# Kernel tuning notes

Hardware: AMD Instinct MI355X
Metric: run time of the kernel (lower is better)

Reference implementation:

```python
import jax, jax.numpy as jnp
import numpy as np

NUM_USERS = 500000
NUM_ITEMS = 500000
EMB_DIM = 64
BATCH = 16384
BN_EPS = 1e-5


def setup_inputs() -> dict:
    key = jax.random.key(0)
    ks = jax.random.split(key, 16)
    d = {}
    d["user_ids"] = jax.random.randint(ks[0], (BATCH,), 0, NUM_USERS)
    d["item_ids"] = jax.random.randint(ks[1], (BATCH,), 0, NUM_ITEMS)
    # wide layer: Linear(num_users+num_items, 1) -> weight stored as a flat vector + scalar bias
    d["wide_w"] = jax.random.normal(ks[2], (NUM_USERS + NUM_ITEMS,), jnp.float32) * 0.002
    d["wide_b"] = jnp.zeros((), jnp.float32)
    # embedding tables (init normal std=0.1 as in _init_weights)
    d["user_table"] = jax.random.normal(ks[3], (NUM_USERS, EMB_DIM), jnp.float32) * 0.1
    d["item_table"] = jax.random.normal(ks[4], (NUM_ITEMS, EMB_DIM), jnp.float32) * 0.1
    # deep MLP: 128 -> 256 -> 128 -> 64 -> 1, xavier-ish init, zero bias
    dims = [2 * EMB_DIM, 256, 128, 64]
    for i, (din, dout) in enumerate(zip(dims[:-1], dims[1:]), start=1):
        scale = float(np.sqrt(6.0 / (din + dout)))
        d[f"w{i}"] = jax.random.uniform(ks[4 + i], (din, dout), jnp.float32, -scale, scale)
        d[f"b{i}"] = jnp.zeros((dout,), jnp.float32)
        d[f"g{i}"] = jnp.ones((dout,), jnp.float32)   # BN gamma
        d[f"be{i}"] = jnp.zeros((dout,), jnp.float32)  # BN beta
    scale = float(np.sqrt(6.0 / (64 + 1)))
    d["w4"] = jax.random.uniform(ks[9], (64, 1), jnp.float32, -scale, scale)
    d["b4"] = jnp.zeros((1,), jnp.float32)
    return d


def _bn_eval(h, g, be):
    # eval-mode BatchNorm1d with running_mean=0, running_var=1
    return g * (h * (1.0 / jnp.sqrt(1.0 + BN_EPS))) + be


def reference(user_ids, item_ids, wide_w, wide_b, user_table, item_table,
              w1, b1, g1, be1, w2, b2, g2, be2, w3, b3, g3, be3, w4, b4):
    # Wide path: one_hot(user) @ W.T + one_hot(item) @ W.T + b  ==  gather + sum + bias
    wide = wide_w[user_ids] + wide_w[NUM_USERS + item_ids] + wide_b  # [B]
    # Deep path
    x = jnp.concatenate([user_table[user_ids], item_table[item_ids]], axis=1)  # [B, 128]
    for w, b, g, be in ((w1, b1, g1, be1), (w2, b2, g2, be2), (w3, b3, g3, be3)):
        x = _bn_eval(jax.nn.relu(x @ w + b), g, be)  # Linear -> ReLU -> BN (Dropout=id in eval)
    deep = (x @ w4 + b4)[:, 0]  # [B]
    return wide + deep
```

## Files before the change

### kernel.cpp

```cpp
#include <hip/hip_runtime.h>


#define NT 512
#define TS 32

constexpr int NUM_USERS = 500000;
constexpr float BN_INV = 0.9999950000374997f;

struct __align__(16) Smem {
    float xs[TS * 132];
    float h1[TS * 260];
};

#define FMA4(xk, wv, a)                      \
    do {                                     \
        (a).x = fmaf((xk), (wv).x, (a).x);   \
        (a).y = fmaf((xk), (wv).y, (a).y);   \
        (a).z = fmaf((xk), (wv).z, (a).z);   \
        (a).w = fmaf((xk), (wv).w, (a).w);   \
    } while (0)

template <int K, int KS, int N, int NS, int FS>
__device__ __forceinline__ void mlp_layer(
    const float* __restrict__ w, const float* __restrict__ bias,
    const float* __restrict__ gamma, const float* __restrict__ beta,
    const float* in_lds, float* out_lds, int t)
{
    constexpr int JG     = FS / 4;
    constexpr int SG     = 64 / JG;
    constexpr int NSLICE = N / FS;
    constexpr int SM     = TS * NSLICE / 8;
    constexpr int SPL    = SM / SG;
    constexpr int NW4    = N / 4;
    static_assert(SPL * SG == SM, "layout");

    const int wave = t >> 6, lane = t & 63;
    const int wslice = wave % NSLICE, wsamp = wave / NSLICE;
    const int jg = lane % JG, sg = lane / JG;
    const int j0 = wslice * FS + jg * 4;
    const int s0 = wsamp * SM + sg * SPL;

    float4 acc[SPL];
#pragma unroll
    for (int s = 0; s < SPL; ++s) acc[s] = make_float4(0.f, 0.f, 0.f, 0.f);

    const float4* wp = (const float4*)w + (j0 >> 2);

#pragma unroll 4
    for (int k4 = 0; k4 < K; k4 += 4) {
        float4 wv0 = wp[(k4 + 0) * NW4];
        float4 wv1 = wp[(k4 + 1) * NW4];
        float4 wv2 = wp[(k4 + 2) * NW4];
        float4 wv3 = wp[(k4 + 3) * NW4];
        float4 xv[SPL];
#pragma unroll
        for (int s = 0; s < SPL; ++s)
            xv[s] = *(const float4*)&in_lds[(s0 + s) * KS + k4];
#pragma unroll
        for (int s = 0; s < SPL; ++s) {
            FMA4(xv[s].x, wv0, acc[s]);
            FMA4(xv[s].y, wv1, acc[s]);
            FMA4(xv[s].z, wv2, acc[s]);
            FMA4(xv[s].w, wv3, acc[s]);
        }
    }

    const float4 bv = *(const float4*)&bias[j0];
    const float4 gv = *(const float4*)&gamma[j0];
    const float4 ev = *(const float4*)&beta[j0];
#pragma unroll
    for (int s = 0; s < SPL; ++s) {
        float4 o;
        o.x = fmaxf(acc[s].x + bv.x, 0.f) * (gv.x * BN_INV) + ev.x;
        o.y = fmaxf(acc[s].y + bv.y, 0.f) * (gv.y * BN_INV) + ev.y;
        o.z = fmaxf(acc[s].z + bv.z, 0.f) * (gv.z * BN_INV) + ev.z;
        o.w = fmaxf(acc[s].w + bv.w, 0.f) * (gv.w * BN_INV) + ev.w;
        *(float4*)&out_lds[(s0 + s) * NS + j0] = o;
    }
}

__global__ __launch_bounds__(NT, 4) void wd_kernel(
    const int* __restrict__ user_ids, const int* __restrict__ item_ids,
    const float* __restrict__ wide_w, const float* __restrict__ wide_b,
    const float* __restrict__ user_table, const float* __restrict__ item_table,
    const float* __restrict__ w1, const float* __restrict__ b1,
    const float* __restrict__ g1, const float* __restrict__ be1,
    const float* __restrict__ w2, const float* __restrict__ b2,
    const float* __restrict__ g2, const float* __restrict__ be2,
    const float* __restrict__ w3, const float* __restrict__ b3,
    const float* __restrict__ g3, const float* __restrict__ be3,
    const float* __restrict__ w4, const float* __restrict__ b4,
    float* __restrict__ out)
{
    __shared__ Smem sm;
    const int t = threadIdx.x;
    const int sbase = blockIdx.x * TS;

    {
        const int s = t >> 4;
        const int p = t & 15;
        const int uid = user_ids[sbase + s];
        const int iid = item_ids[sbase + s];
        float4* row = (float4*)&sm.xs[s * 132];
        row[p]      = ((const float4*)(user_table + (long)uid * 64))[p];
        row[16 + p] = ((const float4*)(item_table + (long)iid * 64))[p];
    }

    float widev = 0.0f;
    if (t < TS * 8 && (t & 7) == 0) {
        const int s = t >> 3;
        const int uid = user_ids[sbase + s];
        const int iid = item_ids[sbase + s];
        widev = wide_w[uid] + wide_w[NUM_USERS + iid] + wide_b[0];
    }
    __syncthreads();

    mlp_layer<128, 132, 256, 260, 64>(w1, b1, g1, be1, sm.xs, sm.h1, t);
    __syncthreads();
    mlp_layer<256, 260, 128, 132, 32>(w2, b2, g2, be2, sm.h1, sm.xs, t);
    __syncthreads();
    mlp_layer<128, 132,  64,  68, 32>(w3, b3, g3, be3, sm.xs, sm.h1, t);
    __syncthreads();

    if (t < TS * 8) {
        const int s = t >> 3;
        const int g = t & 7;
        const float* h = &sm.h1[s * 68 + g * 8];
        const float4 ha = *(const float4*)(h);
        const float4 hb = *(const float4*)(h + 4);
        const float4 wa = *(const float4*)(w4 + g * 8);
        const float4 wb = *(const float4*)(w4 + g * 8 + 4);
        float p = ha.x * wa.x + ha.y * wa.y + ha.z * wa.z + ha.w * wa.w
                + hb.x * wb.x + hb.y * wb.y + hb.z * wb.z + hb.w * wb.w;
        p += __shfl_down(p, 4);
        p += __shfl_down(p, 2);
        p += __shfl_down(p, 1);
        if (g == 0) out[sbase + s] = widev + p + b4[0];
    }
}

extern "C" void kernel_launch(void* const* d_in, const int* in_sizes, int n_in,
                              void* d_out, int out_size, void* d_ws, size_t ws_size,
                              hipStream_t stream) {
    (void)in_sizes; (void)n_in; (void)d_ws; (void)ws_size;
    const int*   user_ids   = (const int*)d_in[0];
    const int*   item_ids   = (const int*)d_in[1];
    const float* wide_w     = (const float*)d_in[2];
    const float* wide_b     = (const float*)d_in[3];
    const float* user_table = (const float*)d_in[4];
    const float* item_table = (const float*)d_in[5];
    const float* w1 = (const float*)d_in[6];
    const float* b1 = (const float*)d_in[7];
    const float* g1 = (const float*)d_in[8];
    const float* be1 = (const float*)d_in[9];
    const float* w2 = (const float*)d_in[10];
    const float* b2 = (const float*)d_in[11];
    const float* g2 = (const float*)d_in[12];
    const float* be2 = (const float*)d_in[13];
    const float* w3 = (const float*)d_in[14];
    const float* b3 = (const float*)d_in[15];
    const float* g3 = (const float*)d_in[16];
    const float* be3 = (const float*)d_in[17];
    const float* w4 = (const float*)d_in[18];
    const float* b4 = (const float*)d_in[19];
    float* out = (float*)d_out;

    const int grid = 16384 / TS;
    wd_kernel<<<grid, NT, 0, stream>>>(
        user_ids, item_ids, wide_w, wide_b, user_table, item_table,
        w1, b1, g1, be1, w2, b2, g2, be2, w3, b3, g3, be3, w4, b4, out);
}
```

Baseline: 310.9 us.

## Halve block tile to 16 samples and software-prefetch weight rows

```diff
diff --git a/kernel.cpp b/kernel.cpp
--- a/kernel.cpp
+++ b/kernel.cpp
@@ -1,8 +1,8 @@
 #include <hip/hip_runtime.h>
 
 
-#define NT 512
-#define TS 32
+#define NT 256
+#define TS 16
 
 constexpr int NUM_USERS = 500000;
 constexpr float BN_INV = 0.9999950000374997f;
@@ -20,25 +20,23 @@
         (a).w = fmaf((xk), (wv).w, (a).w);   \
     } while (0)
 
-template <int K, int KS, int N, int NS, int FS>
+template <int K, int KS, int N, int NS>
 __device__ __forceinline__ void mlp_layer(
     const float* __restrict__ w, const float* __restrict__ bias,
     const float* __restrict__ gamma, const float* __restrict__ beta,
     const float* in_lds, float* out_lds, int t)
 {
-    constexpr int JG     = FS / 4;
-    constexpr int SG     = 64 / JG;
-    constexpr int NSLICE = N / FS;
-    constexpr int SM     = TS * NSLICE / 8;
-    constexpr int SPL    = SM / SG;
-    constexpr int NW4    = N / 4;
-    static_assert(SPL * SG == SM, "layout");
+    constexpr int FS  = N / 4;
+    constexpr int JG  = FS / 4;
+    constexpr int SG  = 64 / JG;
+    constexpr int SPL = TS / SG;
+    constexpr int NW4 = N / 4;
+    static_assert(SPL * SG == TS, "layout");
 
     const int wave = t >> 6, lane = t & 63;
-    const int wslice = wave % NSLICE, wsamp = wave / NSLICE;
     const int jg = lane % JG, sg = lane / JG;
-    const int j0 = wslice * FS + jg * 4;
-    const int s0 = wsamp * SM + sg * SPL;
+    const int j0 = wave * FS + jg * 4;
+    const int s0 = sg * SPL;
 
     float4 acc[SPL];
 #pragma unroll
@@ -46,12 +44,20 @@
 
     const float4* wp = (const float4*)w + (j0 >> 2);
 
-#pragma unroll 4
+    float4 wv0 = wp[0 * NW4];
+    float4 wv1 = wp[1 * NW4];
+    float4 wv2 = wp[2 * NW4];
+    float4 wv3 = wp[3 * NW4];
+
+#pragma unroll 2
     for (int k4 = 0; k4 < K; k4 += 4) {
-        float4 wv0 = wp[(k4 + 0) * NW4];
-        float4 wv1 = wp[(k4 + 1) * NW4];
-        float4 wv2 = wp[(k4 + 2) * NW4];
-        float4 wv3 = wp[(k4 + 3) * NW4];
+        float4 wn0, wn1, wn2, wn3;
+        if (k4 + 4 < K) {
+            wn0 = wp[(k4 + 4) * NW4];
+            wn1 = wp[(k4 + 5) * NW4];
+            wn2 = wp[(k4 + 6) * NW4];
+            wn3 = wp[(k4 + 7) * NW4];
+        }
         float4 xv[SPL];
 #pragma unroll
         for (int s = 0; s < SPL; ++s)
@@ -63,6 +69,7 @@
             FMA4(xv[s].z, wv2, acc[s]);
             FMA4(xv[s].w, wv3, acc[s]);
         }
+        wv0 = wn0; wv1 = wn1; wv2 = wn2; wv3 = wn3;
     }
 
     const float4 bv = *(const float4*)&bias[j0];
@@ -79,7 +86,7 @@
     }
 }
 
-__global__ __launch_bounds__(NT, 4) void wd_kernel(
+__global__ __launch_bounds__(NT, 5) void wd_kernel(
     const int* __restrict__ user_ids, const int* __restrict__ item_ids,
     const float* __restrict__ wide_w, const float* __restrict__ wide_b,
     const float* __restrict__ user_table, const float* __restrict__ item_table,
@@ -115,11 +122,11 @@
     }
     __syncthreads();
 
-    mlp_layer<128, 132, 256, 260, 64>(w1, b1, g1, be1, sm.xs, sm.h1, t);
+    mlp_layer<128, 132, 256, 260>(w1, b1, g1, be1, sm.xs, sm.h1, t);
     __syncthreads();
-    mlp_layer<256, 260, 128, 132, 32>(w2, b2, g2, be2, sm.h1, sm.xs, t);
+    mlp_layer<256, 260, 128, 132>(w2, b2, g2, be2, sm.h1, sm.xs, t);
     __syncthreads();
-    mlp_layer<128, 132,  64,  68, 32>(w3, b3, g3, be3, sm.xs, sm.h1, t);
+    mlp_layer<128, 132,  64,  68>(w3, b3, g3, be3, sm.xs, sm.h1, t);
     __syncthreads();
 
     if (t < TS * 8) {
```

Measured after the change: 307.7 us. Within noise of the previous version (-1.0%).
